# Kernel tuning notes

Measured on AMD Instinct MI355X. Metric: run time of the kernel, lower is better.

## Reference

```python
import jax, jax.numpy as jnp
import numpy as np

B, S, E, H = 2, 2048, 2048, 16
NOPE, ROPE, VD = 128, 64, 128
QH = NOPE + ROPE  # 192
LORA = 512
ROPE_THETA = 10000.0
EPS = 1e-6


def setup_inputs() -> dict:
    key = jax.random.key(0)
    ks = jax.random.split(key, 5)
    sd = lambda n: 1.0 / np.sqrt(n)
    return {
        "x": jax.random.normal(ks[0], (B, S, E), jnp.float32),
        "wq": jax.random.normal(ks[1], (E, H * QH), jnp.float32) * sd(E),
        "wkv_a": jax.random.normal(ks[2], (E, LORA + ROPE), jnp.float32) * sd(E),
        "wkv_b": jax.random.normal(ks[3], (LORA, H * (NOPE + VD)), jnp.float32) * sd(LORA),
        "wo": jax.random.normal(ks[4], (H * VD, E), jnp.float32) * sd(H * VD),
        "kv_norm_scale": jnp.ones((LORA,), jnp.float32),
    }


def _rope(xp, cos, sin):
    # xp: (..., s, d); cos/sin: (s, d//2)
    d2 = xp.shape[-1] // 2
    x1, x2 = xp[..., :d2], xp[..., d2:]
    return jnp.concatenate([x1 * cos - x2 * sin, x2 * cos + x1 * sin], axis=-1)


def reference(x, wq, wkv_a, wkv_b, wo, kv_norm_scale):
    b, s, _ = x.shape
    # queries: (b, H, s, QH), split into no-pe / pe slices
    q = (x @ wq).reshape(b, s, H, QH).transpose(0, 2, 1, 3)
    q_nope, q_pe = q[..., :NOPE], q[..., NOPE:]

    # low-rank KV latent projection
    kva = x @ wkv_a  # (b, s, LORA + ROPE)
    ckv, k_pe = kva[..., :LORA], kva[..., LORA:]
    ckv = ckv * jax.lax.rsqrt(jnp.mean(ckv * ckv, axis=-1, keepdims=True) + EPS)
    ckv = ckv * kv_norm_scale  # RMSNorm on latent
    kv = (ckv @ wkv_b).reshape(b, s, H, NOPE + VD).transpose(0, 2, 1, 3)
    k_nope, v = kv[..., :NOPE], kv[..., NOPE:]

    # partial RoPE on the rope slice only
    pos = jnp.arange(s, dtype=jnp.float32)
    inv = 1.0 / (ROPE_THETA ** (jnp.arange(0, ROPE, 2, dtype=jnp.float32) / ROPE))
    ang = pos[:, None] * inv  # (s, ROPE//2)
    cos, sin = jnp.cos(ang), jnp.sin(ang)
    q_pe = _rope(q_pe, cos, sin)                 # (b, H, s, ROPE)
    k_pe = _rope(k_pe[:, None, :, :], cos, sin)  # (b, 1, s, ROPE), shared over heads

    # concat (the new_empty + slice-write in torch)
    qs = jnp.concatenate([q_nope, q_pe], axis=-1)  # (b, H, s, QH)
    ks_ = jnp.concatenate(
        [k_nope, jnp.broadcast_to(k_pe, (b, H, s, ROPE))], axis=-1
    )  # (b, H, s, QH)

    # causal SDPA with scale = q_head_dim**-0.5; asymmetric V head dim
    scale = QH ** -0.5
    scores = jnp.einsum('bhqd,bhkd->bhqk', qs, ks_) * scale
    causal = jnp.tril(jnp.ones((s, s), dtype=bool))
    scores = jnp.where(causal, scores, jnp.finfo(scores.dtype).min)
    attn = jax.nn.softmax(scores, axis=-1)
    out = jnp.einsum('bhqk,bhkd->bhqd', attn, v)  # (b, H, s, VD)
    out = out.transpose(0, 2, 1, 3).reshape(b, s, H * VD)
    return out @ wo
```

## Files before the change

kernel.cpp:

```cpp
#include <hip/hip_runtime.h>
#include <stdint.h>
#include <stddef.h>

typedef __bf16 bf16x8 __attribute__((ext_vector_type(8)));
typedef float floatx4 __attribute__((ext_vector_type(4)));
typedef unsigned short u16;

__device__ __forceinline__ float bf2f(u16 h) {
    unsigned u = ((unsigned)h) << 16;
    return __builtin_bit_cast(float, u);
}
__device__ __forceinline__ u16 f2bf(float f) {
    unsigned u = __builtin_bit_cast(unsigned, f);
    u += 0x7fffu + ((u >> 16) & 1u);
    return (u16)(u >> 16);
}

__device__ __forceinline__ void gload16(const void* g, void* l) {
    __builtin_amdgcn_global_load_lds(
        (const __attribute__((address_space(1))) uint32_t*)g,
        (__attribute__((address_space(3))) uint32_t*)l, 16, 0, 0);
}

__device__ __forceinline__ void wait_vm8() { asm volatile("s_waitcnt vmcnt(8)" ::: "memory"); }
__device__ __forceinline__ void wait_vm6() { asm volatile("s_waitcnt vmcnt(6)" ::: "memory"); }
__device__ __forceinline__ void wait_vm4() { asm volatile("s_waitcnt vmcnt(4)" ::: "memory"); }
__device__ __forceinline__ void wait_vm3() { asm volatile("s_waitcnt vmcnt(3)" ::: "memory"); }
__device__ __forceinline__ void wait_vm0() { asm volatile("s_waitcnt vmcnt(0)" ::: "memory"); }

__global__ __launch_bounds__(256) void k_conv_x(const float* __restrict__ in,
                                                u16* __restrict__ out, int n8) {
    int i = blockIdx.x * 256 + threadIdx.x;
    if (i >= n8) return;
    const float* f = in + (size_t)i * 8;
    unsigned o[4];
    for (int t = 0; t < 4; t++) {
        u16 lo = f2bf(f[2 * t]), hi = f2bf(f[2 * t + 1]);
        o[t] = (unsigned)lo | ((unsigned)hi << 16);
    }
    uint4 p = {o[0], o[1], o[2], o[3]};
    *(uint4*)&out[(size_t)i * 8] = p;
}

__global__ __launch_bounds__(256) void k_convT(const float* __restrict__ in,
                                               u16* __restrict__ out, int K, int N) {
    __shared__ u16 t[32][33];
    int k0 = blockIdx.x * 32, n0 = blockIdx.y * 32;
    int c = threadIdx.x & 31, r8 = threadIdx.x >> 5;
    for (int j = 0; j < 4; j++) {
        int row = r8 + j * 8;
        int n = n0 + c;
        t[row][c] = (n < N) ? f2bf(in[(size_t)(k0 + row) * N + n]) : (u16)0;
    }
    __syncthreads();
    for (int j = 0; j < 4; j++) {
        int row = r8 + j * 8;
        out[(size_t)(n0 + row) * K + k0 + c] = t[c][row];
    }
}

__global__ __launch_bounds__(256) void k_transpose_v(const u16* __restrict__ kv,
                                                     u16* __restrict__ vt) {
    __shared__ u16 t[32][33];
    int bh = blockIdx.z;
    int s0 = blockIdx.x * 32, v0 = blockIdx.y * 32;
    int c = threadIdx.x & 31, r8 = threadIdx.x >> 5;
    int b = bh >> 4, h = bh & 15;
    for (int j = 0; j < 4; j++) {
        int s = s0 + r8 + j * 8;
        t[r8 + j * 8][c] = kv[(size_t)(b * 2048 + s) * 4096 + h * 256 + 128 + v0 + c];
    }
    __syncthreads();
    for (int j = 0; j < 4; j++) {
        int v = v0 + r8 + j * 8;
        vt[((size_t)bh * 128 + v) * 2048 + s0 + c] = t[c][r8 + j * 8];
    }
}

template <int NWC, int MODE>
__global__ __launch_bounds__(512, 2) void k_gemm256(const u16* __restrict__ A,
                                                    const u16* __restrict__ BT,
                                                    void* __restrict__ C0,
                                                    void* __restrict__ C1,
                                                    int K, int ldc) {
    constexpr int MFR = 16 / (8 / NWC);
    constexpr int ACH = 2;
    constexpr int BCH = NWC / 2;
    constexpr int SLOT = 8192 + NWC * 2048;
    __shared__ __align__(16) u16 RING[4][SLOT];
    int tid = threadIdx.x;
    int w = tid >> 6, lane = tid & 63;
    int l15 = lane & 15, quad = lane >> 4;
    int wr = w / NWC, wc = w % NWC;

    int gx = gridDim.x;
    int nwg = gx * gridDim.y;
    int flat = blockIdx.y * gx + blockIdx.x;
    int cpx = nwg >> 3;
    int swz = (flat & 7) * cpx + (flat >> 3);
    int bx = swz % gx, by = swz / gx;
    size_t m0 = (size_t)bx * 256, n0 = (size_t)by * (NWC * 64);
    int NT = K >> 5;

    const u16* srcA[ACH];
    const u16* srcB[BCH];
    int ldsAb[ACH], ldsBb[BCH];
#pragma unroll
    for (int p = 0; p < ACH; p++) {
        int chunk = p * 512 + tid;
        int s = chunk >> 6;
        int b = (chunk & 63) * 8;
        int bu = b ^ (((b >> 8) & 1) << 4);
        int r = bu >> 5, c = bu & 31;
        srcA[p] = A + (m0 + s * 16 + r) * (size_t)K + c;
        ldsAb[p] = (p * 512 + w * 64) * 8;
    }
#pragma unroll
    for (int p = 0; p < BCH; p++) {
        int chunk = p * 512 + tid;
        int s = chunk >> 6;
        int b = (chunk & 63) * 8;
        int bu = b ^ (((b >> 8) & 1) << 4);
        int r = bu >> 5, c = bu & 31;
        srcB[p] = BT + (n0 + s * 16 + r) * (size_t)K + c;
        ldsBb[p] = 8192 + (p * 512 + w * 64) * 8;
    }

    const int swb = (l15 * 32 + quad * 8) ^ ((l15 >> 3) << 4);

    floatx4 acc[MFR][4];
    const floatx4 fzero = {0.f, 0.f, 0.f, 0.f};
#pragma unroll
    for (int i = 0; i < MFR; i++)
#pragma unroll
        for (int j = 0; j < 4; j++) acc[i][j] = fzero;

    bf16x8 aA[MFR], bB[4];

    auto STAGE = [&](int j) {
        int rs = j & 3;
        size_t ko = (size_t)j * 32;
        u16* ring = &RING[rs][0];
#pragma unroll
        for (int p = 0; p < ACH; p++) gload16(srcA[p] + ko, ring + ldsAb[p]);
#pragma unroll
        for (int p = 0; p < BCH; p++) gload16(srcB[p] + ko, ring + ldsBb[p]);
    };
    auto READ = [&](int rs) {
        const u16* ring = &RING[rs][0];
#pragma unroll
        for (int i2 = 0; i2 < MFR; i2++)
            aA[i2] = *(const bf16x8*)&ring[(wr * MFR + i2) * 512 + swb];
#pragma unroll
        for (int j2 = 0; j2 < 4; j2++)
            bB[j2] = *(const bf16x8*)&ring[8192 + (wc * 4 + j2) * 512 + swb];
    };
    auto MMA = [&]() {
        __builtin_amdgcn_s_setprio(1);
#pragma unroll
        for (int i2 = 0; i2 < MFR; i2++)
#pragma unroll
            for (int j2 = 0; j2 < 4; j2++)
                acc[i2][j2] = __builtin_amdgcn_mfma_f32_16x16x32_bf16(
                    aA[i2], bB[j2], acc[i2][j2], 0, 0, 0);
        __builtin_amdgcn_s_setprio(0);
    };

    STAGE(0); STAGE(1); STAGE(2);

    int j = 0;
    for (; j + 3 < NT; j++) {
        if constexpr (NWC == 4) wait_vm8(); else wait_vm6();
        __builtin_amdgcn_s_barrier();
        __builtin_amdgcn_sched_barrier(0);
        READ(j & 3);
        STAGE(j + 3);
        __builtin_amdgcn_sched_barrier(0);
        MMA();
    }
    {
        if constexpr (NWC == 4) wait_vm8(); else wait_vm6();
        __builtin_amdgcn_s_barrier();
        __builtin_amdgcn_sched_barrier(0);
        READ(j & 3); MMA(); j++;
    }
    {
        if constexpr (NWC == 4) wait_vm4(); else wait_vm3();
        __builtin_amdgcn_s_barrier();
        __builtin_amdgcn_sched_barrier(0);
        READ(j & 3); MMA(); j++;
    }
    {
        wait_vm0();
        __builtin_amdgcn_s_barrier();
        __builtin_amdgcn_sched_barrier(0);
        READ(j & 3); MMA();
    }

#pragma unroll
    for (int i = 0; i < MFR; i++)
#pragma unroll
        for (int j2 = 0; j2 < 4; j2++) {
            size_t col = n0 + wc * 64 + j2 * 16 + l15;
#pragma unroll
            for (int r = 0; r < 4; r++) {
                size_t row = m0 + (size_t)wr * (MFR * 16) + i * 16 + quad * 4 + r;
                if constexpr (MODE == 0) {
                    ((u16*)C0)[row * ldc + col] = f2bf(acc[i][j2][r]);
                } else if constexpr (MODE == 1) {
                    ((float*)C0)[row * ldc + col] = acc[i][j2][r];
                } else {
                    if (col < 3072)
                        ((u16*)C0)[row * 3072 + col] = f2bf(acc[i][j2][r]);
                    else if (col < 3648)
                        ((u16*)C1)[row * 576 + (col - 3072)] = f2bf(acc[i][j2][r]);
                }
            }
        }
}

__global__ __launch_bounds__(64) void k_rmsnorm(const u16* __restrict__ kva,
                                                const float* __restrict__ scl,
                                                u16* __restrict__ ckv) {
    int r = blockIdx.x, lane = threadIdx.x;
    const u16* row = kva + (size_t)r * 576 + lane * 8;
    uint4 raw = *(const uint4*)row;
    unsigned w[4] = {raw.x, raw.y, raw.z, raw.w};
    float f[8];
    float ss = 0.f;
    for (int t = 0; t < 4; t++) {
        f[2 * t]     = bf2f((u16)(w[t] & 0xffffu));
        f[2 * t + 1] = bf2f((u16)(w[t] >> 16));
        ss += f[2 * t] * f[2 * t] + f[2 * t + 1] * f[2 * t + 1];
    }
    for (int off = 1; off < 64; off <<= 1) ss += __shfl_xor(ss, off, 64);
    float rs = rsqrtf(ss * (1.f / 512.f) + 1e-6f);
    unsigned o[4];
    for (int t = 0; t < 4; t++) {
        u16 lo = f2bf(f[2 * t] * rs * scl[lane * 8 + 2 * t]);
        u16 hi = f2bf(f[2 * t + 1] * rs * scl[lane * 8 + 2 * t + 1]);
        o[t] = (unsigned)lo | ((unsigned)hi << 16);
    }
    uint4 packed = {o[0], o[1], o[2], o[3]};
    *(uint4*)(ckv + (size_t)r * 512 + lane * 8) = packed;
}

__global__ __launch_bounds__(256) void k_rope(u16* __restrict__ qbuf, u16* __restrict__ kva) {
    int tid = threadIdx.x;
    int rloc = tid >> 7;
    int task = tid & 127;
    int r = blockIdx.x * 2 + rloc;
    __shared__ float cs_s[2][32], sn_s[2][32];
    if (tid < 64) {
        int rr = tid >> 5, i = tid & 31;
        int ss = (blockIdx.x * 2 + rr) & 2047;
        float freq = __expf(-0.28782313662425575f * (float)i);
        float ang = (float)ss * freq;
        float sn, cs;
        sincosf(ang, &sn, &cs);
        cs_s[rr][i] = cs; sn_s[rr][i] = sn;
    }
    __syncthreads();
    if (task < 68) {
        int rb = task >> 2, q = task & 3;
        u16* base = (rb < 16) ? qbuf + (size_t)r * 3072 + rb * 192 + 128
                              : kva + (size_t)r * 576 + 512;
        u16* p1 = base + q * 8;
        uint4 x1v = *(uint4*)p1;
        uint4 x2v = *(uint4*)(p1 + 32);
        unsigned w1[4] = {x1v.x, x1v.y, x1v.z, x1v.w};
        unsigned w2[4] = {x2v.x, x2v.y, x2v.z, x2v.w};
        unsigned o1[4], o2[4];
        for (int t2 = 0; t2 < 4; t2++) {
            float a1 = bf2f((u16)(w1[t2] & 0xffffu)), b1 = bf2f((u16)(w1[t2] >> 16));
            float a2 = bf2f((u16)(w2[t2] & 0xffffu)), b2 = bf2f((u16)(w2[t2] >> 16));
            int i0 = q * 8 + t2 * 2, i1 = i0 + 1;
            float c0 = cs_s[rloc][i0], s0 = sn_s[rloc][i0];
            float c1 = cs_s[rloc][i1], s1 = sn_s[rloc][i1];
            o1[t2] = (unsigned)f2bf(a1 * c0 - a2 * s0) | ((unsigned)f2bf(b1 * c1 - b2 * s1) << 16);
            o2[t2] = (unsigned)f2bf(a2 * c0 + a1 * s0) | ((unsigned)f2bf(b2 * c1 + b1 * s1) << 16);
        }
        uint4 y1 = {o1[0], o1[1], o1[2], o1[3]};
        uint4 y2 = {o2[0], o2[1], o2[2], o2[3]};
        *(uint4*)p1 = y1;
        *(uint4*)(p1 + 32) = y2;
    }
}

__global__ __launch_bounds__(256, 3) void k_attn(const u16* __restrict__ qbuf,
                                                 const u16* __restrict__ kv,
                                                 const u16* __restrict__ kva,
                                                 const u16* __restrict__ vt,
                                                 u16* __restrict__ attno) {
    int tid = threadIdx.x;
    int wave = tid >> 6, lane = tid & 63;
    int quad = lane >> 4, l15 = lane & 15;
    int hb = blockIdx.x;
    int h = hb & 15, b = hb >> 4;
    int qb = 31 - (int)blockIdx.y;
    int qg0 = qb * 64 + wave * 16;
    int row = qg0 + l15;

    __shared__ __align__(16) u16 Kn[2][32 * 136];
    __shared__ __align__(16) u16 Kp[2][32 * 72];
    __shared__ __align__(16) u16 Vs[2][128 * 40];
    __shared__ __align__(16) u16 P[4][16 * 40];

    const u16* qrp = qbuf + ((size_t)(b * 2048) + qg0 + l15) * 3072 + h * 192;
    bf16x8 qf[6];
    for (int c = 0; c < 6; c++) qf[c] = *(const bf16x8*)&qrp[c * 32 + quad * 8];

    const floatx4 fzero = {0.f, 0.f, 0.f, 0.f};
    floatx4 o[8];
    for (int f = 0; f < 8; f++) o[f] = fzero;
    float lp = 0.f;

    const u16* kvb = kv  + (size_t)(b * 2048) * 4096 + h * 256;
    const u16* kpb = kva + (size_t)(b * 2048) * 576 + 512;
    const u16* vtb = vt  + (size_t)(b * 16 + h) * 128 * 2048;
    const float scale = 0.07216878364870323f;

    int nkt = qb * 2 + 2;

    int kKey0 = tid >> 4,          kOff0 = (tid & 15) * 8;
    int kKey1 = (tid + 256) >> 4,  kOff1 = (tid & 15) * 8;
    int pKey  = tid >> 3,          pOff  = (tid & 7) * 8;
    int vRow0 = tid >> 2,          vOff0 = (tid & 3) * 8;
    int vRow1 = (tid + 256) >> 2,  vOff1 = (tid & 3) * 8;

    {
        uint4 a = *(const uint4*)&kvb[(size_t)kKey0 * 4096 + kOff0];
        uint4 c = *(const uint4*)&kvb[(size_t)kKey1 * 4096 + kOff1];
        uint4 d = *(const uint4*)&kpb[(size_t)pKey * 576 + pOff];
        uint4 e = *(const uint4*)&vtb[(size_t)vRow0 * 2048 + vOff0];
        uint4 g = *(const uint4*)&vtb[(size_t)vRow1 * 2048 + vOff1];
        *(uint4*)&Kn[0][kKey0 * 136 + kOff0] = a;
        *(uint4*)&Kn[0][kKey1 * 136 + kOff1] = c;
        *(uint4*)&Kp[0][pKey * 72 + pOff] = d;
        *(uint4*)&Vs[0][vRow0 * 40 + vOff0] = e;
        *(uint4*)&Vs[0][vRow1 * 40 + vOff1] = g;
    }
    __syncthreads();

    for (int kt = 0; kt < nkt; kt++) {
        int cur = kt & 1;
        bool have = (kt + 1) < nkt;
        uint4 sA = {}, sB = {}, sC = {}, sD = {}, sE = {};
        if (have) {
            int kb = (kt + 1) * 32;
            sA = *(const uint4*)&kvb[(size_t)(kb + kKey0) * 4096 + kOff0];
            sB = *(const uint4*)&kvb[(size_t)(kb + kKey1) * 4096 + kOff1];
            sC = *(const uint4*)&kpb[(size_t)(kb + pKey) * 576 + pOff];
            sD = *(const uint4*)&vtb[(size_t)vRow0 * 2048 + kb + vOff0];
            sE = *(const uint4*)&vtb[(size_t)vRow1 * 2048 + kb + vOff1];
        }
        if (kt * 32 <= qg0 + 15) {
            bf16x8 vf[8];
            for (int f = 0; f < 8; f++)
                vf[f] = *(const bf16x8*)&Vs[cur][(f * 16 + l15) * 40 + quad * 8];
            floatx4 sc[2] = {fzero, fzero};
            __builtin_amdgcn_s_setprio(1);
            for (int hf = 0; hf < 2; hf++) {
                const u16* kn = &Kn[cur][(hf * 16 + l15) * 136];
                const u16* kp = &Kp[cur][(hf * 16 + l15) * 72];
                for (int c = 0; c < 4; c++) {
                    bf16x8 kf = *(const bf16x8*)&kn[c * 32 + quad * 8];
                    sc[hf] = __builtin_amdgcn_mfma_f32_16x16x32_bf16(kf, qf[c], sc[hf], 0, 0, 0);
                }
                for (int c = 0; c < 2; c++) {
                    bf16x8 kf = *(const bf16x8*)&kp[c * 32 + quad * 8];
                    sc[hf] = __builtin_amdgcn_mfma_f32_16x16x32_bf16(kf, qf[4 + c], sc[hf], 0, 0, 0);
                }
            }
            __builtin_amdgcn_s_setprio(0);
            asm volatile("" ::: "memory");
            for (int hf = 0; hf < 2; hf++) {
                int keyb = kt * 32 + hf * 16 + quad * 4;
                float p[4];
                for (int r = 0; r < 4; r++)
                    p[r] = (keyb + r <= row) ? __expf(sc[hf][r] * scale) : 0.f;
                lp += (p[0] + p[1]) + (p[2] + p[3]);
                unsigned d0 = (unsigned)f2bf(p[0]) | ((unsigned)f2bf(p[1]) << 16);
                unsigned d1 = (unsigned)f2bf(p[2]) | ((unsigned)f2bf(p[3]) << 16);
                uint2 pk = {d0, d1};
                *(uint2*)&P[wave][l15 * 40 + hf * 16 + quad * 4] = pk;
            }
            asm volatile("" ::: "memory");
            bf16x8 pa = *(const bf16x8*)&P[wave][l15 * 40 + quad * 8];
            asm volatile("" ::: "memory");
            __builtin_amdgcn_s_setprio(1);
            for (int f = 0; f < 8; f++)
                o[f] = __builtin_amdgcn_mfma_f32_16x16x32_bf16(pa, vf[f], o[f], 0, 0, 0);
            __builtin_amdgcn_s_setprio(0);
        }
        if (have) {
            int nb = cur ^ 1;
            *(uint4*)&Kn[nb][kKey0 * 136 + kOff0] = sA;
            *(uint4*)&Kn[nb][kKey1 * 136 + kOff1] = sB;
            *(uint4*)&Kp[nb][pKey * 72 + pOff] = sC;
            *(uint4*)&Vs[nb][vRow0 * 40 + vOff0] = sD;
            *(uint4*)&Vs[nb][vRow1 * 40 + vOff1] = sE;
        }
        __syncthreads();
    }

    lp += __shfl_xor(lp, 16, 64);
    lp += __shfl_xor(lp, 32, 64);
    float lrow[4];
    for (int r = 0; r < 4; r++) lrow[r] = __shfl(lp, quad * 4 + r, 64);
    for (int f = 0; f < 8; f++)
        for (int r = 0; r < 4; r++) {
            int orow = qg0 + quad * 4 + r;
            float val = o[f][r] / lrow[r];
            attno[((size_t)(b * 2048) + orow) * 2048 + h * 128 + f * 16 + l15] = f2bf(val);
        }
}

extern "C" void kernel_launch(void* const* d_in, const int* in_sizes, int n_in,
                              void* d_out, int out_size, void* d_ws, size_t ws_size,
                              hipStream_t stream) {
    const float* x_raw    = (const float*)d_in[0];
    const float* wq_raw   = (const float*)d_in[1];
    const float* wkva_raw = (const float*)d_in[2];
    const float* wkvb_raw = (const float*)d_in[3];
    const float* wo_raw   = (const float*)d_in[4];
    const float* kvs_raw  = (const float*)d_in[5];
    float* out = (float*)d_out;
    u16* ws = (u16*)d_ws;

    const size_t O_ATT = 0;
    const size_t O_VT  = 8388608;
    const size_t O_QB  = 16777216;
    const size_t O_KVA = 29360128;
    const size_t O_KV  = 31719424;
    const size_t TOTAL_BYTES = 48496640ull * 2;
    if (ws_size < TOTAL_BYTES) return;

    u16* g12bt  = ws + O_ATT;
    u16* ckv    = ws + O_ATT;
    u16* wkvb_t = ws + O_ATT + 2097152;
    u16* attno  = ws + O_ATT;
    u16* x_bf   = ws + O_VT;
    u16* vt     = ws + O_VT;
    u16* qbuf   = ws + O_QB;
    u16* wo_t   = ws + O_QB;
    u16* kva    = ws + O_KVA;
    u16* kv     = ws + O_KV;

    k_conv_x<<<4096, 256, 0, stream>>>(x_raw, x_bf, 1048576);
    k_convT<<<dim3(64, 96), 256, 0, stream>>>(wq_raw, g12bt, 2048, 3072);
    k_convT<<<dim3(64, 20), 256, 0, stream>>>(wkva_raw, g12bt + (size_t)3072 * 2048, 2048, 576);

    k_gemm256<2, 2><<<dim3(16, 29), 512, 0, stream>>>(x_bf, g12bt, qbuf, kva, 2048, 0);

    k_rmsnorm<<<4096, 64, 0, stream>>>(kva, kvs_raw, ckv);
    k_convT<<<dim3(16, 128), 256, 0, stream>>>(wkvb_raw, wkvb_t, 512, 4096);
    k_gemm256<4, 0><<<dim3(16, 16), 512, 0, stream>>>(ckv, wkvb_t, kv, nullptr, 512, 4096);

    k_rope<<<2048, 256, 0, stream>>>(qbuf, kva);
    k_transpose_v<<<dim3(64, 4, 32), 256, 0, stream>>>(kv, vt);

    k_attn<<<dim3(32, 32), 256, 0, stream>>>(qbuf, kv, kva, vt, attno);

    k_convT<<<dim3(64, 64), 256, 0, stream>>>(wo_raw, wo_t, 2048, 2048);
    k_gemm256<2, 1><<<dim3(16, 16), 512, 0, stream>>>(attno, wo_t, out, nullptr, 2048, 2048);
}
```

Baseline: 397.0 us.

## Fuse V transpose into kv GEMM epilogue and read K directly from global

The kv projection GEMM gains an epilogue mode that writes the K-nope half row-major and the V half directly in transposed (b,h,vd,s) layout, so the separate V transpose kernel is removed. The attention kernel also stops staging K-nope and K-rope tiles in shared memory and loads the K fragments per lane straight from global memory before the score MFMAs. This removes a kernel launch and a round trip through memory for V, and frees LDS, which may help occupancy. The cost is strided 8-byte scattered stores in the GEMM epilogue, and global-load latency exposed inside the attention inner loop, because K is no longer prefetched.

```diff
diff --git a/kernel.cpp b/kernel.cpp
--- a/kernel.cpp
+++ b/kernel.cpp
@@ -56,24 +56,6 @@
     for (int j = 0; j < 4; j++) {
         int row = r8 + j * 8;
         out[(size_t)(n0 + row) * K + k0 + c] = t[c][row];
-    }
-}
-
-__global__ __launch_bounds__(256) void k_transpose_v(const u16* __restrict__ kv,
-                                                     u16* __restrict__ vt) {
-    __shared__ u16 t[32][33];
-    int bh = blockIdx.z;
-    int s0 = blockIdx.x * 32, v0 = blockIdx.y * 32;
-    int c = threadIdx.x & 31, r8 = threadIdx.x >> 5;
-    int b = bh >> 4, h = bh & 15;
-    for (int j = 0; j < 4; j++) {
-        int s = s0 + r8 + j * 8;
-        t[r8 + j * 8][c] = kv[(size_t)(b * 2048 + s) * 4096 + h * 256 + 128 + v0 + c];
-    }
-    __syncthreads();
-    for (int j = 0; j < 4; j++) {
-        int v = v0 + r8 + j * 8;
-        vt[((size_t)bh * 128 + v) * 2048 + s0 + c] = t[c][r8 + j * 8];
     }
 }
 
@@ -209,11 +191,27 @@
                     ((u16*)C0)[row * ldc + col] = f2bf(acc[i][j2][r]);
                 } else if constexpr (MODE == 1) {
                     ((float*)C0)[row * ldc + col] = acc[i][j2][r];
-                } else {
+                } else if constexpr (MODE == 2) {
                     if (col < 3072)
                         ((u16*)C0)[row * 3072 + col] = f2bf(acc[i][j2][r]);
                     else if (col < 3648)
                         ((u16*)C1)[row * 576 + (col - 3072)] = f2bf(acc[i][j2][r]);
+                }
+            }
+            if constexpr (MODE == 3) {
+                int cm = (int)(col & 255);
+                size_t row0 = m0 + (size_t)wr * (MFR * 16) + i * 16 + quad * 4;
+                if (cm < 128) {
+#pragma unroll
+                    for (int r = 0; r < 4; r++)
+                        ((u16*)C0)[(row0 + r) * 4096 + col] = f2bf(acc[i][j2][r]);
+                } else {
+                    int h = (int)(col >> 8), vd = cm - 128;
+                    size_t b = row0 >> 11, s = row0 & 2047;
+                    unsigned lo = (unsigned)f2bf(acc[i][j2][0]) | ((unsigned)f2bf(acc[i][j2][1]) << 16);
+                    unsigned hi = (unsigned)f2bf(acc[i][j2][2]) | ((unsigned)f2bf(acc[i][j2][3]) << 16);
+                    uint2 pk = {lo, hi};
+                    *(uint2*)&((u16*)C1)[(((b << 4) + h) * 128 + vd) * 2048 + s] = pk;
                 }
             }
         }
@@ -301,8 +299,6 @@
     int qg0 = qb * 64 + wave * 16;
     int row = qg0 + l15;
 
-    __shared__ __align__(16) u16 Kn[2][32 * 136];
-    __shared__ __align__(16) u16 Kp[2][32 * 72];
     __shared__ __align__(16) u16 Vs[2][128 * 40];
     __shared__ __align__(16) u16 P[4][16 * 40];
 
@@ -322,21 +318,12 @@
 
     int nkt = qb * 2 + 2;
 
-    int kKey0 = tid >> 4,          kOff0 = (tid & 15) * 8;
-    int kKey1 = (tid + 256) >> 4,  kOff1 = (tid & 15) * 8;
-    int pKey  = tid >> 3,          pOff  = (tid & 7) * 8;
     int vRow0 = tid >> 2,          vOff0 = (tid & 3) * 8;
     int vRow1 = (tid + 256) >> 2,  vOff1 = (tid & 3) * 8;
 
     {
-        uint4 a = *(const uint4*)&kvb[(size_t)kKey0 * 4096 + kOff0];
-        uint4 c = *(const uint4*)&kvb[(size_t)kKey1 * 4096 + kOff1];
-        uint4 d = *(const uint4*)&kpb[(size_t)pKey * 576 + pOff];
         uint4 e = *(const uint4*)&vtb[(size_t)vRow0 * 2048 + vOff0];
         uint4 g = *(const uint4*)&vtb[(size_t)vRow1 * 2048 + vOff1];
-        *(uint4*)&Kn[0][kKey0 * 136 + kOff0] = a;
-        *(uint4*)&Kn[0][kKey1 * 136 + kOff1] = c;
-        *(uint4*)&Kp[0][pKey * 72 + pOff] = d;
         *(uint4*)&Vs[0][vRow0 * 40 + vOff0] = e;
         *(uint4*)&Vs[0][vRow1 * 40 + vOff1] = g;
     }
@@ -345,12 +332,9 @@
     for (int kt = 0; kt < nkt; kt++) {
         int cur = kt & 1;
         bool have = (kt + 1) < nkt;
-        uint4 sA = {}, sB = {}, sC = {}, sD = {}, sE = {};
+        uint4 sD = {}, sE = {};
         if (have) {
             int kb = (kt + 1) * 32;
-            sA = *(const uint4*)&kvb[(size_t)(kb + kKey0) * 4096 + kOff0];
-            sB = *(const uint4*)&kvb[(size_t)(kb + kKey1) * 4096 + kOff1];
-            sC = *(const uint4*)&kpb[(size_t)(kb + pKey) * 576 + pOff];
             sD = *(const uint4*)&vtb[(size_t)vRow0 * 2048 + kb + vOff0];
             sE = *(const uint4*)&vtb[(size_t)vRow1 * 2048 + kb + vOff1];
         }
@@ -359,20 +343,17 @@
             for (int f = 0; f < 8; f++)
                 vf[f] = *(const bf16x8*)&Vs[cur][(f * 16 + l15) * 40 + quad * 8];
             floatx4 sc[2] = {fzero, fzero};
-            __builtin_amdgcn_s_setprio(1);
             for (int hf = 0; hf < 2; hf++) {
-                const u16* kn = &Kn[cur][(hf * 16 + l15) * 136];
-                const u16* kp = &Kp[cur][(hf * 16 + l15) * 72];
-                for (int c = 0; c < 4; c++) {
-                    bf16x8 kf = *(const bf16x8*)&kn[c * 32 + quad * 8];
-                    sc[hf] = __builtin_amdgcn_mfma_f32_16x16x32_bf16(kf, qf[c], sc[hf], 0, 0, 0);
-                }
-                for (int c = 0; c < 2; c++) {
-                    bf16x8 kf = *(const bf16x8*)&kp[c * 32 + quad * 8];
-                    sc[hf] = __builtin_amdgcn_mfma_f32_16x16x32_bf16(kf, qf[4 + c], sc[hf], 0, 0, 0);
-                }
+                const u16* kn = kvb + (size_t)(kt * 32 + hf * 16 + l15) * 4096;
+                const u16* kp = kpb + (size_t)(kt * 32 + hf * 16 + l15) * 576;
+                bf16x8 kfr[6];
+                for (int c = 0; c < 4; c++) kfr[c]     = *(const bf16x8*)&kn[c * 32 + quad * 8];
+                for (int c = 0; c < 2; c++) kfr[4 + c] = *(const bf16x8*)&kp[c * 32 + quad * 8];
+                __builtin_amdgcn_s_setprio(1);
+                for (int c = 0; c < 6; c++)
+                    sc[hf] = __builtin_amdgcn_mfma_f32_16x16x32_bf16(kfr[c], qf[c], sc[hf], 0, 0, 0);
+                __builtin_amdgcn_s_setprio(0);
             }
-            __builtin_amdgcn_s_setprio(0);
             asm volatile("" ::: "memory");
             for (int hf = 0; hf < 2; hf++) {
                 int keyb = kt * 32 + hf * 16 + quad * 4;
@@ -395,9 +376,6 @@
         }
         if (have) {
             int nb = cur ^ 1;
-            *(uint4*)&Kn[nb][kKey0 * 136 + kOff0] = sA;
-            *(uint4*)&Kn[nb][kKey1 * 136 + kOff1] = sB;
-            *(uint4*)&Kp[nb][pKey * 72 + pOff] = sC;
             *(uint4*)&Vs[nb][vRow0 * 40 + vOff0] = sD;
             *(uint4*)&Vs[nb][vRow1 * 40 + vOff1] = sE;
         }
@@ -455,10 +433,9 @@
 
     k_rmsnorm<<<4096, 64, 0, stream>>>(kva, kvs_raw, ckv);
     k_convT<<<dim3(16, 128), 256, 0, stream>>>(wkvb_raw, wkvb_t, 512, 4096);
-    k_gemm256<4, 0><<<dim3(16, 16), 512, 0, stream>>>(ckv, wkvb_t, kv, nullptr, 512, 4096);
+    k_gemm256<4, 3><<<dim3(16, 16), 512, 0, stream>>>(ckv, wkvb_t, kv, vt, 512, 4096);
 
     k_rope<<<2048, 256, 0, stream>>>(qbuf, kva);
-    k_transpose_v<<<dim3(64, 4, 32), 256, 0, stream>>>(kv, vt);
 
     k_attn<<<dim3(32, 32), 256, 0, stream>>>(qbuf, kv, kva, vt, attno);
 
```

Result: slower. 510.6 us (+28.6%).
